# Performance work log

Measured on AMD Instinct MI355X. Metric: run time of the kernel, lower is better.

## Reference

```python
import jax, jax.numpy as jnp
import numpy as np

N, NC, D, K = 262144, 4096, 5, 4   # fine dof, coarse dof, nnz/row of A, interp points/row of P
W = 2.0 / 3.0                      # weighted-Jacobi weight
PRE, POST, COARSE = 3, 3, 10       # smoothing counts from the source


def setup_inputs() -> dict:
    key = jax.random.key(0)
    k1, k2, k3, k4, k5 = jax.random.split(key, 5)
    # A in ELL form: slot 0 is the diagonal, made strictly diagonally dominant.
    acols_off = jax.random.randint(k1, (N, D - 1), 0, N)
    A_cols = jnp.concatenate([jnp.arange(N)[:, None], acols_off], axis=1).astype(jnp.int32)
    off = -jax.random.uniform(k2, (N, D - 1), dtype=jnp.float32)          # negative off-diagonals (M-matrix-like)
    diag = 2.0 + jnp.sum(jnp.abs(off), axis=1)
    A_vals = jnp.concatenate([diag[:, None], off], axis=1)
    # P in ELL form: slot 0 maps fine node i -> coarse node i // (N//NC) so every coarse dof is covered.
    pcols_off = jax.random.randint(k3, (N, K - 1), 0, NC)
    P_cols = jnp.concatenate([(jnp.arange(N) // (N // NC))[:, None], pcols_off], axis=1).astype(jnp.int32)
    P_vals = jax.random.uniform(k4, (N, K), dtype=jnp.float32) * 0.5
    b = jax.random.normal(k5, (N,), dtype=jnp.float32)
    x = jnp.zeros((N,), dtype=jnp.float32)
    return {"b": b, "x": x, "A_vals": A_vals, "P_vals": P_vals,
            "A_cols": A_cols, "P_cols": P_cols, "num": 2}


def _spmv(vals, cols, x):
    # ELL SpMV: y[i] = sum_d vals[i,d] * x[cols[i,d]]
    return jnp.sum(vals * x[cols], axis=1)


def _jacobi_ell(vals, cols, diag, b, x, n):
    def step(xc, _):
        return xc + W * (b - _spmv(vals, cols, xc)) / diag, None
    x, _ = jax.lax.scan(step, x, None, length=n)
    return x


def _rap(A_vals, A_cols, P_vals, P_cols):
    # A_c = P^T A P, assembled densely on the coarse level via one big scatter-add.
    Pj_vals = P_vals[A_cols]                                   # [N,D,K]
    Pj_cols = P_cols[A_cols]                                   # [N,D,K]
    vals = (P_vals[:, None, :, None] * A_vals[:, :, None, None]
            * Pj_vals[:, :, None, :])                          # [N,D,K,K]
    a_idx = jnp.broadcast_to(P_cols[:, None, :, None].astype(jnp.int32), (N, D, K, K))
    b_idx = jnp.broadcast_to(Pj_cols[:, :, None, :].astype(jnp.int32), (N, D, K, K))
    flat = (a_idx * NC + b_idx).reshape(-1)
    Ac = jax.ops.segment_sum(vals.reshape(-1), flat, num_segments=NC * NC)
    return Ac.reshape(NC, NC)


def reference(b, x, A_vals, P_vals, A_cols, P_cols, num):
    diag_f = A_vals[:, 0]                      # fine-level diagonal (slot 0)
    Ac = _rap(A_vals, A_cols, P_vals, P_cols)  # coarse operator R A P
    diag_c = jnp.diag(Ac)

    def coarse_solve(bc):
        def step(xc, _):
            return xc + W * (bc - Ac @ xc) / diag_c, None
        xc, _ = jax.lax.scan(step, jnp.zeros((NC,), bc.dtype), None, length=COARSE)
        return xc

    for _ in range(num):                       # mg.Iterate, `num` V-cycles
        x = _jacobi_ell(A_vals, A_cols, diag_f, b, x, PRE)          # pre-smooth
        r = b - _spmv(A_vals, A_cols, x)                            # residual
        bc = jax.ops.segment_sum((P_vals * r[:, None]).reshape(-1),  # restrict: R r = P^T r
                                 P_cols.reshape(-1), num_segments=NC)
        xc = coarse_solve(bc)                                       # coarse Jacobi solve
        x = x + jnp.sum(P_vals * xc[P_cols], axis=1)                # prolongate correction
        x = _jacobi_ell(A_vals, A_cols, diag_f, b, x, POST)         # post-smooth
    return x
```

## Files before the change

kernel.cpp:

```cpp
#include <hip/hip_runtime.h>
#include <hip/hip_fp16.h>

#define NN 262144
#define NCC 4096
#define DD 5
#define PRE_IT 3
#define POST_IT 3
#define COARSE_IT 10
#define WJ ((float)(2.0/3.0))
#define NBLK 256
#define BAR_SLOT_U32 768
#define BAR_SLOTS 40
#define POISON 0xAAAAAAAAu
#define BASE_SUM 0x55555540u

typedef unsigned long long u64;

__device__ __forceinline__ unsigned pack_ch(unsigned col, float v) {
  return col | ((unsigned)__half_as_ushort(__float2half(v)) << 16);
}
__device__ __forceinline__ float unpack_h(unsigned w) {
  return __half2float(__ushort_as_half((unsigned short)(w >> 16)));
}

__device__ __forceinline__ float ldA(const float* p) {
  return __hip_atomic_load(p, __ATOMIC_RELAXED, __HIP_MEMORY_SCOPE_AGENT);
}
__device__ __forceinline__ void stA(float* p, float v) {
  __hip_atomic_store(p, v, __ATOMIC_RELAXED, __HIP_MEMORY_SCOPE_AGENT);
}
__device__ __forceinline__ unsigned ldAu(const unsigned* p) {
  return __hip_atomic_load(p, __ATOMIC_RELAXED, __HIP_MEMORY_SCOPE_AGENT);
}
__device__ __forceinline__ void stAu(unsigned* p, unsigned v) {
  __hip_atomic_store(p, v, __ATOMIC_RELAXED, __HIP_MEMORY_SCOPE_AGENT);
}
__device__ __forceinline__ u64 ldA64(const u64* p) {
  return __hip_atomic_load(p, __ATOMIC_RELAXED, __HIP_MEMORY_SCOPE_AGENT);
}
__device__ __forceinline__ void stA64(u64* p, u64 v) {
  __hip_atomic_store(p, v, __ATOMIC_RELAXED, __HIP_MEMORY_SCOPE_AGENT);
}

__device__ __forceinline__ void gbar(unsigned* bar, int& bs, int* sflag) {
  __syncthreads();
  if (threadIdx.x == 0) {
    unsigned* slot  = bar + bs * BAR_SLOT_U32;
    unsigned* line  = slot + ((blockIdx.x & 31) << 4);
    unsigned* flags = slot + 512;
    unsigned r = __hip_atomic_fetch_add(line, 1u, __ATOMIC_RELAXED,
                                        __HIP_MEMORY_SCOPE_AGENT);
    if ((blockIdx.x & 31) == 0 && r == POISON + 7u) {
      for (;;) {
        unsigned s = 0;
#pragma unroll
        for (int i = 0; i < 32; ++i) s += ldAu(slot + (i << 4));
        if (s - BASE_SUM >= 256u) break;
        __builtin_amdgcn_s_sleep(1);
      }
#pragma unroll
      for (int f = 0; f < 16; ++f) stAu(flags + (f << 4), POISON + 1u);
    }
    const unsigned* fl = flags + ((blockIdx.x & 15) << 4);
    while (ldAu(fl) == POISON) __builtin_amdgcn_s_sleep(1);
    __hip_atomic_store(sflag, bs + 1, __ATOMIC_RELAXED, __HIP_MEMORY_SCOPE_WORKGROUP);
  } else if ((threadIdx.x & 63) == 0) {
    while (__hip_atomic_load(sflag, __ATOMIC_RELAXED, __HIP_MEMORY_SCOPE_WORKGROUP) <= bs)
      __builtin_amdgcn_s_sleep(1);
  }
  ++bs;
}

__global__ __launch_bounds__(1024, 4) void k_all(
    const float* __restrict__ b, const float* __restrict__ x_in,
    const float* __restrict__ A_vals, const float* __restrict__ P_vals,
    const int* __restrict__ A_cols, const int* __restrict__ P_cols,
    const int* __restrict__ num_p,
    unsigned* histG, unsigned* offsG, u64* pairs8,
    unsigned* Y, unsigned* tot,
    unsigned* bar, float* partials, float* x2,
    float* xcA, float* xcB, float* out) {
  extern __shared__ char smem[];
  __shared__ float wdiag[16];
  __shared__ float bcl[16];
  __shared__ int sflag;

  const int tid = threadIdx.x;
  const int blk = blockIdx.x;
  const int g = (blk << 10) + tid;
  int bs = 0;
  if (tid == 0) sflag = 0;

  const int4* pc4 = (const int4*)P_cols;
  const float4* pv4 = (const float4*)P_vals;
  unsigned* base_t = histG;

  {
    unsigned* s1 = (unsigned*)smem;
    unsigned* s2 = s1 + NCC;
    unsigned* s3 = s2 + NCC;
    unsigned* sv = s3 + NCC;

    const int4 pc = pc4[g];
    const float4 pv = pv4[g];

    for (int q = tid; q < NCC; q += 1024) s1[q] = 0u;
    __syncthreads();
    {
      int ac[DD]; float av[DD];
#pragma unroll
      for (int j = 0; j < DD; ++j) { ac[j] = A_cols[g * DD + j]; av[j] = A_vals[g * DD + j]; }
      u64* yp = (u64*)(Y + 20u * (unsigned)g);
#pragma unroll
      for (int j = 0; j < DD; ++j) {
        const int4 pcn = pc4[ac[j]];
        const float4 pvn = pv4[ac[j]];
        const u64 lo = (u64)pack_ch((unsigned)pcn.x, av[j] * pvn.x)
                     | ((u64)pack_ch((unsigned)pcn.y, av[j] * pvn.y) << 32);
        const u64 hi = (u64)pack_ch((unsigned)pcn.z, av[j] * pvn.z)
                     | ((u64)pack_ch((unsigned)pcn.w, av[j] * pvn.w) << 32);
        stA64(yp + 2 * j, lo);
        stA64(yp + 2 * j + 1, hi);
      }
    }
    atomicAdd(&s1[pc.x], 1u); atomicAdd(&s1[pc.y], 1u);
    atomicAdd(&s1[pc.z], 1u); atomicAdd(&s1[pc.w], 1u);
    __syncthreads();
    for (int q = tid; q < NCC; q += 1024) stAu(&histG[(blk << 12) + q], s1[q]);
    gbar(bar, bs, &sflag);

    {
      const int w = tid >> 6, l = tid & 63;
      const int c = (blk << 4) + w;
      const unsigned h0 = ldAu(&histG[(((l << 2) + 0) << 12) + c]);
      const unsigned h1 = ldAu(&histG[(((l << 2) + 1) << 12) + c]);
      const unsigned h2 = ldAu(&histG[(((l << 2) + 2) << 12) + c]);
      const unsigned h3 = ldAu(&histG[(((l << 2) + 3) << 12) + c]);
      const unsigned s = h0 + h1 + h2 + h3;
      unsigned scan = s;
#pragma unroll
      for (int d = 1; d < 64; d <<= 1) {
        unsigned v = __shfl_up(scan, d);
        if (l >= d) scan += v;
      }
      const unsigned pre = scan - s;
      stAu(&base_t[(((l << 2) + 0) << 12) + c], pre);
      stAu(&base_t[(((l << 2) + 1) << 12) + c], pre + h0);
      stAu(&base_t[(((l << 2) + 2) << 12) + c], pre + h0 + h1);
      stAu(&base_t[(((l << 2) + 3) << 12) + c], pre + h0 + h1 + h2);
      if (l == 63) stAu(&tot[c], scan);
    }
    gbar(bar, bs, &sflag);

    {
      for (int q = tid; q < NCC; q += 1024) s1[q] = ldAu(&tot[q]);
      __syncthreads();
      const unsigned a0 = s1[(tid << 2) + 0], a1 = s1[(tid << 2) + 1],
                     a2 = s1[(tid << 2) + 2], a3 = s1[(tid << 2) + 3];
      const unsigned tsum = a0 + a1 + a2 + a3;
      sv[tid] = tsum; __syncthreads();
      for (int off = 1; off < 1024; off <<= 1) {
        unsigned v = (tid >= off) ? sv[tid - off] : 0u;
        __syncthreads();
        sv[tid] += v;
        __syncthreads();
      }
      const unsigned excl = sv[tid] - tsum;
      s1[(tid << 2) + 0] = excl;
      s1[(tid << 2) + 1] = excl + a0;
      s1[(tid << 2) + 2] = excl + a0 + a1;
      s1[(tid << 2) + 3] = excl + a0 + a1 + a2;
      __syncthreads();
      if (tid < 16) stAu(&offsG[(blk << 4) + tid], s1[(blk << 4) + tid]);
      if (blk == 255 && tid == 1023) stAu(&offsG[NCC], excl + tsum);
      for (int q = tid; q < NCC; q += 1024)
        s2[q] = s1[q] + ldAu(&base_t[(blk << 12) + q]);
      for (int q = tid; q < NCC; q += 1024) s3[q] = 0u;
      __syncthreads();
      unsigned r;
      r = atomicAdd(&s3[pc.x], 1u);
      stA64(&pairs8[s2[pc.x] + r], (u64)(unsigned)g | ((u64)__float_as_uint(pv.x) << 32));
      r = atomicAdd(&s3[pc.y], 1u);
      stA64(&pairs8[s2[pc.y] + r], (u64)(unsigned)g | ((u64)__float_as_uint(pv.y) << 32));
      r = atomicAdd(&s3[pc.z], 1u);
      stA64(&pairs8[s2[pc.z] + r], (u64)(unsigned)g | ((u64)__float_as_uint(pv.z) << 32));
      r = atomicAdd(&s3[pc.w], 1u);
      stA64(&pairs8[s2[pc.w] + r], (u64)(unsigned)g | ((u64)__float_as_uint(pv.w) << 32));
    }
    gbar(bar, bs, &sflag);
  }

  __half* slab  = (__half*)smem;
  float* rowbuf = (float*)(smem + 131072);

  for (int rr = 0; rr < 16; ++rr) {
    const int c1 = (blk << 4) + rr;
    for (int q = tid; q < NCC; q += 1024) rowbuf[q] = 0.f;
    __syncthreads();
    const unsigned p0 = ldAu(&offsG[c1]), p1 = ldAu(&offsG[c1 + 1]);
    for (unsigned p = p0 + tid; p < p1; p += 1024) {
      const u64 e = ldA64(&pairs8[p]);
      const float pvf = __uint_as_float((unsigned)(e >> 32));
      const u64* yp = (const u64*)(Y + 20u * (unsigned)(e & 0xffffffffu));
      u64 y0 = ldA64(yp + 0), y1 = ldA64(yp + 1), y2 = ldA64(yp + 2), y3 = ldA64(yp + 3),
          y4 = ldA64(yp + 4), y5 = ldA64(yp + 5), y6 = ldA64(yp + 6), y7 = ldA64(yp + 7),
          y8 = ldA64(yp + 8), y9 = ldA64(yp + 9);
#define SCAT(yk) { \
      const unsigned lo_ = (unsigned)(yk), hi_ = (unsigned)((yk) >> 32); \
      atomicAdd(&rowbuf[lo_ & 0xffffu], pvf * unpack_h(lo_)); \
      atomicAdd(&rowbuf[hi_ & 0xffffu], pvf * unpack_h(hi_)); }
      SCAT(y0) SCAT(y1) SCAT(y2) SCAT(y3) SCAT(y4)
      SCAT(y5) SCAT(y6) SCAT(y7) SCAT(y8) SCAT(y9)
#undef SCAT
    }
    __syncthreads();
    if (tid == 0) wdiag[rr] = WJ / rowbuf[c1];
    for (int q = tid; q < NCC; q += 1024) slab[(rr << 12) + q] = __float2half(rowbuf[q]);
    __syncthreads();
  }

  const int num = num_p[0];
  if (num <= 0) { stA(out + g, x_in[g]); return; }

  float av[DD]; int ac[DD];
#pragma unroll
  for (int j = 0; j < DD; ++j) { av[j] = A_vals[g * DD + j]; ac[j] = A_cols[g * DD + j]; }
  const float bg = b[g];
  const float wdg = WJ / av[0];
  const int4 pcg = pc4[g];
  const float4 pvg = pv4[g];
  float xown = x_in[g];

  const float* xr = x_in;
  int wi = 0;

  for (int cyc = 0; cyc < num; ++cyc) {
    for (int it = 0; it < PRE_IT; ++it) {
      float s = av[0] * xown;
#pragma unroll
      for (int j = 1; j < DD; ++j) s += av[j] * ldA(xr + ac[j]);
      const float xn = xown + (bg - s) * wdg;
      float* wb = (wi == 0) ? x2 : out;
      stA(wb + g, xn);
      xown = xn; xr = wb; wi ^= 1;
      gbar(bar, bs, &sflag);
    }
    {
      float s = av[0] * xown;
#pragma unroll
      for (int j = 1; j < DD; ++j) s += av[j] * ldA(xr + ac[j]);
      const float r = bg - s;
      for (int q = tid; q < NCC; q += 1024) rowbuf[q] = 0.f;
      __syncthreads();
      atomicAdd(&rowbuf[pcg.x], pvg.x * r);
      atomicAdd(&rowbuf[pcg.y], pvg.y * r);
      atomicAdd(&rowbuf[pcg.z], pvg.z * r);
      atomicAdd(&rowbuf[pcg.w], pvg.w * r);
      __syncthreads();
      for (int q = tid; q < NCC; q += 1024) stA(&partials[(blk << 12) + q], rowbuf[q]);
      gbar(bar, bs, &sflag);
    }
    {
      const int t2 = tid >> 2;
      const u64* pp = (const u64*)&partials[(t2 << 12) + (blk << 4)];
      const int qq = (tid & 3) << 1;
      const u64 va = ldA64(pp + qq);
      const u64 vb = ldA64(pp + qq + 1);
      ((u64*)rowbuf)[(t2 << 3) + qq] = va;
      ((u64*)rowbuf)[(t2 << 3) + qq + 1] = vb;
      __syncthreads();
      if (tid < 16) {
        float sum = 0.f;
#pragma unroll 8
        for (int t3 = 0; t3 < 256; ++t3) sum += rowbuf[(t3 << 4) + tid];
        bcl[tid] = sum;
        stA(&xcA[(blk << 4) + tid], sum * wdiag[tid]);
      }
      gbar(bar, bs, &sflag);
    }
    const float* xc_cur = xcA;
    float* xc_nxt = xcB;
    for (int it = 1; it < COARSE_IT; ++it) {
      const int w = tid >> 6, l = tid & 63;
      const int xb = (w << 8) + (l << 2);
      const u64* xp = (const u64*)(xc_cur + xb);
      const u64 xlo = ldA64(xp), xhi = ldA64(xp + 1);
      float4 xv;
      xv.x = __uint_as_float((unsigned)xlo); xv.y = __uint_as_float((unsigned)(xlo >> 32));
      xv.z = __uint_as_float((unsigned)xhi); xv.w = __uint_as_float((unsigned)(xhi >> 32));
      float acc[16];
#pragma unroll
      for (int r2 = 0; r2 < 16; ++r2) {
        const __half2* hp2 = (const __half2*)(slab + (r2 << 12) + (w << 8) + (l << 2));
        const float2 f01 = __half22float2(hp2[0]);
        const float2 f23 = __half22float2(hp2[1]);
        acc[r2] = f01.x * xv.x + f01.y * xv.y + f23.x * xv.z + f23.y * xv.w;
      }
#pragma unroll
      for (int r2 = 0; r2 < 16; ++r2) {
        float v = acc[r2];
        v += __shfl_down(v, 32); v += __shfl_down(v, 16); v += __shfl_down(v, 8);
        v += __shfl_down(v, 4);  v += __shfl_down(v, 2);  v += __shfl_down(v, 1);
        acc[r2] = v;
      }
      if (l == 0) {
#pragma unroll
        for (int r2 = 0; r2 < 16; ++r2) rowbuf[(w << 4) + r2] = acc[r2];
      }
      __syncthreads();
      if (tid < 16) {
        float y = 0.f;
#pragma unroll
        for (int w2 = 0; w2 < 16; ++w2) y += rowbuf[(w2 << 4) + tid];
        const float xo = ldA(xc_cur + (blk << 4) + tid);
        stA(&xc_nxt[(blk << 4) + tid], xo + (bcl[tid] - y) * wdiag[tid]);
      }
      float* tmp = (float*)xc_cur; xc_cur = xc_nxt; xc_nxt = tmp;
      gbar(bar, bs, &sflag);
    }
    {
      const u64* xq = (const u64*)(xc_cur + (tid << 2));
      const u64 qa = ldA64(xq), qb = ldA64(xq + 1);
      ((u64*)rowbuf)[(tid << 1)] = qa;
      ((u64*)rowbuf)[(tid << 1) + 1] = qb;
      __syncthreads();
      float* xw = (float*)xr;
      const float corr = pvg.x * rowbuf[pcg.x] + pvg.y * rowbuf[pcg.y] +
                         pvg.z * rowbuf[pcg.z] + pvg.w * rowbuf[pcg.w];
      const float xn = xown + corr;
      stA(xw + g, xn);
      xown = xn;
      gbar(bar, bs, &sflag);
    }
    for (int it = 0; it < POST_IT; ++it) {
      float s = av[0] * xown;
#pragma unroll
      for (int j = 1; j < DD; ++j) s += av[j] * ldA(xr + ac[j]);
      const float xn = xown + (bg - s) * wdg;
      float* wb = (wi == 0) ? x2 : out;
      stA(wb + g, xn);
      xown = xn; xr = wb; wi ^= 1;
      if (!(cyc == num - 1 && it == POST_IT - 1)) gbar(bar, bs, &sflag);
    }
  }
}

extern "C" void kernel_launch(void* const* d_in, const int* in_sizes, int n_in,
                              void* d_out, int out_size, void* d_ws, size_t ws_size,
                              hipStream_t stream) {
  (void)in_sizes; (void)n_in; (void)out_size; (void)ws_size;
  const float* b      = (const float*)d_in[0];
  const float* x_in   = (const float*)d_in[1];
  const float* A_vals = (const float*)d_in[2];
  const float* P_vals = (const float*)d_in[3];
  const int*   A_cols = (const int*)d_in[4];
  const int*   P_cols = (const int*)d_in[5];
  const int*   num_p  = (const int*)d_in[6];
  float* out = (float*)d_out;

  char* ws = (char*)d_ws;
  unsigned* offsG  = (unsigned*)(ws + 0);
  unsigned* tot    = (unsigned*)(ws + 20480);
  float*    xcA    = (float*)(ws + 40960);
  float*    xcB    = (float*)(ws + 57344);
  unsigned* bar    = (unsigned*)(ws + 73728);
  u64*      pairs8 = (u64*)(ws + 262144);
  unsigned* histG  = (unsigned*)(ws + 8650752);
  unsigned* Y      = (unsigned*)(ws + 12845056);
  float* partials  = (float*)Y;
  float* x2        = (float*)histG;


  const unsigned smem_bytes = 131072 + 16384;
  hipFuncSetAttribute((const void*)k_all,
                      hipFuncAttributeMaxDynamicSharedMemorySize, (int)smem_bytes);
  hipLaunchKernelGGL(k_all, dim3(NBLK), dim3(1024), smem_bytes, stream,
                     b, x_in, A_vals, P_vals, A_cols, P_cols, num_p,
                     histG, offsG, pairs8, Y, tot,
                     bar, partials, x2, xcA, xcB, out);
}
```

Baseline: 553.4 us.

## Remove grid barriers via global atomic restriction, fused first coarse step, inline prolongation

Restriction now accumulates straight into a global coarse RHS with atomics, replacing per-block partial histograms and the transpose reduction. The first two coarse Jacobi iterations are merged into one barrier phase using a global weighted diagonal. The prolongation store and its grid barrier are dropped by recomputing each neighbour's correction inside the first post-smooth step. This removes roughly three grid-wide barriers per V-cycle, at the cost of global atomic contention and extra gathers of neighbour P rows.

```diff
diff --git a/kernel.cpp b/kernel.cpp
--- a/kernel.cpp
+++ b/kernel.cpp
@@ -78,11 +78,12 @@
     const int* __restrict__ num_p,
     unsigned* histG, unsigned* offsG, u64* pairs8,
     unsigned* Y, unsigned* tot,
-    unsigned* bar, float* partials, float* x2,
+    unsigned* bar, float* bcG, float* wdiagG, float* x2,
     float* xcA, float* xcB, float* out) {
   extern __shared__ char smem[];
   __shared__ float wdiag[16];
   __shared__ float bcl[16];
+  __shared__ float red[256];
   __shared__ int sflag;
 
   const int tid = threadIdx.x;
@@ -192,6 +193,8 @@
 
   __half* slab  = (__half*)smem;
   float* rowbuf = (float*)(smem + 131072);
+
+  if (tid < 16) stA(&bcG[(blk << 4) + tid], 0.f);
 
   for (int rr = 0; rr < 16; ++rr) {
     const int c1 = (blk << 4) + rr;
@@ -214,7 +217,11 @@
 #undef SCAT
     }
     __syncthreads();
-    if (tid == 0) wdiag[rr] = WJ / rowbuf[c1];
+    if (tid == 0) {
+      const float wd = WJ / rowbuf[c1];
+      wdiag[rr] = wd;
+      stA(&wdiagG[c1], wd);
+    }
     for (int q = tid; q < NCC; q += 1024) slab[(rr << 12) + q] = __float2half(rowbuf[q]);
     __syncthreads();
   }
@@ -250,37 +257,63 @@
 #pragma unroll
       for (int j = 1; j < DD; ++j) s += av[j] * ldA(xr + ac[j]);
       const float r = bg - s;
-      for (int q = tid; q < NCC; q += 1024) rowbuf[q] = 0.f;
-      __syncthreads();
-      atomicAdd(&rowbuf[pcg.x], pvg.x * r);
-      atomicAdd(&rowbuf[pcg.y], pvg.y * r);
-      atomicAdd(&rowbuf[pcg.z], pvg.z * r);
-      atomicAdd(&rowbuf[pcg.w], pvg.w * r);
-      __syncthreads();
-      for (int q = tid; q < NCC; q += 1024) stA(&partials[(blk << 12) + q], rowbuf[q]);
+      atomicAdd(&bcG[pcg.x], pvg.x * r);
+      atomicAdd(&bcG[pcg.y], pvg.y * r);
+      atomicAdd(&bcG[pcg.z], pvg.z * r);
+      atomicAdd(&bcG[pcg.w], pvg.w * r);
       gbar(bar, bs, &sflag);
     }
     {
-      const int t2 = tid >> 2;
-      const u64* pp = (const u64*)&partials[(t2 << 12) + (blk << 4)];
-      const int qq = (tid & 3) << 1;
-      const u64 va = ldA64(pp + qq);
-      const u64 vb = ldA64(pp + qq + 1);
-      ((u64*)rowbuf)[(t2 << 3) + qq] = va;
-      ((u64*)rowbuf)[(t2 << 3) + qq + 1] = vb;
+      const int q4 = tid << 2;
+      const u64* bp = (const u64*)(bcG + q4);
+      const u64 b0 = ldA64(bp), b1 = ldA64(bp + 1);
+      const u64* wp = (const u64*)(wdiagG + q4);
+      const u64 w0 = ldA64(wp), w1 = ldA64(wp + 1);
+      float4 y1;
+      y1.x = __uint_as_float((unsigned)b0)         * __uint_as_float((unsigned)w0);
+      y1.y = __uint_as_float((unsigned)(b0 >> 32)) * __uint_as_float((unsigned)(w0 >> 32));
+      y1.z = __uint_as_float((unsigned)b1)         * __uint_as_float((unsigned)w1);
+      y1.w = __uint_as_float((unsigned)(b1 >> 32)) * __uint_as_float((unsigned)(w1 >> 32));
+      ((float4*)rowbuf)[tid] = y1;
+      if (tid < 16) bcl[tid] = ldA(bcG + (blk << 4) + tid);
+      __syncthreads();
+      const int w = tid >> 6, l = tid & 63;
+      const int xb = (w << 8) + (l << 2);
+      const float4 xv = *(const float4*)(rowbuf + xb);
+      float xo_own = 0.f;
+      if (tid < 16) xo_own = rowbuf[(blk << 4) + tid];
+      float acc[16];
+#pragma unroll
+      for (int r2 = 0; r2 < 16; ++r2) {
+        const __half2* hp2 = (const __half2*)(slab + (r2 << 12) + xb);
+        const float2 f01 = __half22float2(hp2[0]);
+        const float2 f23 = __half22float2(hp2[1]);
+        acc[r2] = f01.x * xv.x + f01.y * xv.y + f23.x * xv.z + f23.y * xv.w;
+      }
+#pragma unroll
+      for (int r2 = 0; r2 < 16; ++r2) {
+        float v = acc[r2];
+        v += __shfl_down(v, 32); v += __shfl_down(v, 16); v += __shfl_down(v, 8);
+        v += __shfl_down(v, 4);  v += __shfl_down(v, 2);  v += __shfl_down(v, 1);
+        acc[r2] = v;
+      }
+      if (l == 0) {
+#pragma unroll
+        for (int r2 = 0; r2 < 16; ++r2) red[(w << 4) + r2] = acc[r2];
+      }
       __syncthreads();
       if (tid < 16) {
-        float sum = 0.f;
-#pragma unroll 8
-        for (int t3 = 0; t3 < 256; ++t3) sum += rowbuf[(t3 << 4) + tid];
-        bcl[tid] = sum;
-        stA(&xcA[(blk << 4) + tid], sum * wdiag[tid]);
+        float yy = 0.f;
+#pragma unroll
+        for (int w2 = 0; w2 < 16; ++w2) yy += red[(w2 << 4) + tid];
+        stA(&xcA[(blk << 4) + tid], xo_own + (bcl[tid] - yy) * wdiag[tid]);
       }
       gbar(bar, bs, &sflag);
     }
     const float* xc_cur = xcA;
     float* xc_nxt = xcB;
-    for (int it = 1; it < COARSE_IT; ++it) {
+    for (int it = 2; it < COARSE_IT; ++it) {
+      if (it == 2 && tid < 16) stA(&bcG[(blk << 4) + tid], 0.f);
       const int w = tid >> 6, l = tid & 63;
       const int xb = (w << 8) + (l << 2);
       const u64* xp = (const u64*)(xc_cur + xb);
@@ -291,7 +324,7 @@
       float acc[16];
 #pragma unroll
       for (int r2 = 0; r2 < 16; ++r2) {
-        const __half2* hp2 = (const __half2*)(slab + (r2 << 12) + (w << 8) + (l << 2));
+        const __half2* hp2 = (const __half2*)(slab + (r2 << 12) + xb);
         const float2 f01 = __half22float2(hp2[0]);
         const float2 f23 = __half22float2(hp2[1]);
         acc[r2] = f01.x * xv.x + f01.y * xv.y + f23.x * xv.z + f23.y * xv.w;
@@ -305,15 +338,15 @@
       }
       if (l == 0) {
 #pragma unroll
-        for (int r2 = 0; r2 < 16; ++r2) rowbuf[(w << 4) + r2] = acc[r2];
+        for (int r2 = 0; r2 < 16; ++r2) red[(w << 4) + r2] = acc[r2];
       }
       __syncthreads();
       if (tid < 16) {
-        float y = 0.f;
-#pragma unroll
-        for (int w2 = 0; w2 < 16; ++w2) y += rowbuf[(w2 << 4) + tid];
+        float yy = 0.f;
+#pragma unroll
+        for (int w2 = 0; w2 < 16; ++w2) yy += red[(w2 << 4) + tid];
         const float xo = ldA(xc_cur + (blk << 4) + tid);
-        stA(&xc_nxt[(blk << 4) + tid], xo + (bcl[tid] - y) * wdiag[tid]);
+        stA(&xc_nxt[(blk << 4) + tid], xo + (bcl[tid] - yy) * wdiag[tid]);
       }
       float* tmp = (float*)xc_cur; xc_cur = xc_nxt; xc_nxt = tmp;
       gbar(bar, bs, &sflag);
@@ -324,18 +357,27 @@
       ((u64*)rowbuf)[(tid << 1)] = qa;
       ((u64*)rowbuf)[(tid << 1) + 1] = qb;
       __syncthreads();
-      float* xw = (float*)xr;
       const float corr = pvg.x * rowbuf[pcg.x] + pvg.y * rowbuf[pcg.y] +
                          pvg.z * rowbuf[pcg.z] + pvg.w * rowbuf[pcg.w];
-      const float xn = xown + corr;
-      stA(xw + g, xn);
-      xown = xn;
-      gbar(bar, bs, &sflag);
+      xown = xown + corr;
     }
     for (int it = 0; it < POST_IT; ++it) {
       float s = av[0] * xown;
-#pragma unroll
-      for (int j = 1; j < DD; ++j) s += av[j] * ldA(xr + ac[j]);
+      if (it == 0) {
+#pragma unroll
+        for (int j = 1; j < DD; ++j) {
+          const int aj = ac[j];
+          const int4 pcn = pc4[aj];
+          const float4 pvn = pv4[aj];
+          const float xj = ldA(xr + aj)
+              + pvn.x * rowbuf[pcn.x] + pvn.y * rowbuf[pcn.y]
+              + pvn.z * rowbuf[pcn.z] + pvn.w * rowbuf[pcn.w];
+          s += av[j] * xj;
+        }
+      } else {
+#pragma unroll
+        for (int j = 1; j < DD; ++j) s += av[j] * ldA(xr + ac[j]);
+      }
       const float xn = xown + (bg - s) * wdg;
       float* wb = (wi == 0) ? x2 : out;
       stA(wb + g, xn);
@@ -364,10 +406,11 @@
   float*    xcA    = (float*)(ws + 40960);
   float*    xcB    = (float*)(ws + 57344);
   unsigned* bar    = (unsigned*)(ws + 73728);
+  float*    bcG    = (float*)(ws + 196608);
+  float*    wdiagG = (float*)(ws + 212992);
   u64*      pairs8 = (u64*)(ws + 262144);
   unsigned* histG  = (unsigned*)(ws + 8650752);
   unsigned* Y      = (unsigned*)(ws + 12845056);
-  float* partials  = (float*)Y;
   float* x2        = (float*)histG;
 
 
@@ -377,5 +420,5 @@
   hipLaunchKernelGGL(k_all, dim3(NBLK), dim3(1024), smem_bytes, stream,
                      b, x_in, A_vals, P_vals, A_cols, P_cols, num_p,
                      histG, offsG, pairs8, Y, tot,
-                     bar, partials, x2, xcA, xcB, out);
-}
+                     bar, bcG, wdiagG, x2, xcA, xcB, out);
+}
```

New measurement: 764.6 us. 1.38x slower.
